# Kernel tuning notes

Measured on AMD Instinct MI355X. Metric: run time of the kernel, lower is better.

## Reference

```python
import jax, jax.numpy as jnp
import numpy as np

T, N, E, NNZ, F, D = 8, 50000, 5000, 100000, 128, 128


def setup_inputs() -> dict:
    key = jax.random.key(0)
    ks = jax.random.split(key, 5)
    x = jax.random.normal(ks[0], (T, N, F), jnp.float32)
    pair_nodes = jax.random.randint(ks[1], (T, NNZ), 0, N)
    pair_edges = jax.random.randint(ks[2], (T, NNZ), 0, E)
    W0 = jax.random.normal(ks[3], (F, D), jnp.float32) / np.sqrt(F).astype(np.float32)
    b0 = jnp.zeros((D,), jnp.float32)
    W1 = jax.random.normal(ks[4], (D, D), jnp.float32) / np.sqrt(D).astype(np.float32)
    b1 = jnp.zeros((D,), jnp.float32)
    return {"x": x, "W0": W0, "b0": b0, "W1": W1, "b1": b1,
            "pair_nodes": pair_nodes, "pair_edges": pair_edges}


def _smooth(x, pn, pe):
    """HGNN Laplacian smoothing: D_v^{-1/2} H D_e^{-1} H^T D_v^{-1/2} x.

    x: [N, D]; pn/pe: [NNZ] incidence pairs (node idx, hyperedge idx).
    """
    ones = jnp.ones(pn.shape, x.dtype)
    dv = jax.ops.segment_sum(ones, pn, num_segments=N)  # node degree
    de = jax.ops.segment_sum(ones, pe, num_segments=E)  # hyperedge degree
    dv_safe = jnp.where(dv > 0, dv, 1.0)
    de_safe = jnp.where(de > 0, de, 1.0)
    dv_isqrt = jnp.where(dv > 0, jax.lax.rsqrt(dv_safe), 0.0)
    de_inv = jnp.where(de > 0, 1.0 / de_safe, 0.0)
    xs = x * dv_isqrt[:, None]
    # node -> hyperedge gather/aggregate
    ef = jax.ops.segment_sum(xs[pn], pe, num_segments=E) * de_inv[:, None]
    # hyperedge -> node gather/scatter
    return jax.ops.segment_sum(ef[pe], pn, num_segments=N) * dv_isqrt[:, None]


def reference(x, W0, b0, W1, b1, pair_nodes, pair_edges):
    def step(xt, pn, pe):
        h = jax.nn.relu(_smooth(xt @ W0 + b0, pn, pe))   # layer 0
        h = jax.nn.relu(_smooth(h @ W1 + b1, pn, pe))    # layer 1
        return h.mean(axis=0)                            # mean pool over nodes
    tokens = jax.vmap(step)(x, pair_nodes, pair_edges)   # [T, D]
    return tokens[None]                                  # [1, T, D]
```

## Files before the change

kernel.cpp:

```cpp
#include <hip/hip_runtime.h>

#define TT  8
#define NN  50000
#define EE  5000
#define NZ  100000
#define DD  128
#define ETILES ((EE + 63) / 64)
#define NCAP 16
#define NCH 8
#define CDIV 6250
#define CCAP 16
#define LSTR 136

typedef __attribute__((ext_vector_type(8))) short short8v;
typedef __attribute__((ext_vector_type(4))) float float4v;

__device__ __forceinline__ unsigned short f2bf(float f) {
    return __builtin_bit_cast(unsigned short, (__bf16)f);
}
__device__ __forceinline__ float bf2f(unsigned short u) {
    return (float)__builtin_bit_cast(__bf16, u);
}
__device__ __forceinline__ unsigned short f2h(float f) {
    return __builtin_bit_cast(unsigned short, (_Float16)f);
}
__device__ __forceinline__ float h2f(unsigned short u) {
    return (float)__builtin_bit_cast(_Float16, u);
}

__global__ __launch_bounds__(256) void k_build(const int* __restrict__ pn, const int* __restrict__ pe,
                                               int* __restrict__ dvcnt, int* __restrict__ ccnt,
                                               unsigned short* __restrict__ ell_n,
                                               unsigned short* __restrict__ ell_ec) {
    const int t = blockIdx.x & 7;
    const int i0 = (blockIdx.x >> 3) * 1024 + threadIdx.x;
    int nv[4], ev[4];
    #pragma unroll
    for (int q = 0; q < 4; q++) {
        int i = i0 + q * 256;
        nv[q] = (i < NZ) ? pn[(size_t)t * NZ + i] : -1;
        ev[q] = (i < NZ) ? pe[(size_t)t * NZ + i] : 0;
    }
    for (int c = 0; c < NCH; c++) {
        #pragma unroll
        for (int q = 0; q < 4; q++) {
            int n = nv[q];
            if (n >= 0 && (n / CDIV) == c) {
                int e = ev[q];
                int sn = atomicAdd(&dvcnt[(size_t)t * NN + n], 1);
                if (sn < NCAP) ell_n[((size_t)t * NN + n) * NCAP + sn] = (unsigned short)e;
                int sc = atomicAdd(&ccnt[((size_t)t * EE + e) * NCH + c], 1);
                if (sc < CCAP)
                    ell_ec[(((size_t)t * EE + e) * NCH + c) * CCAP + sc] = (unsigned short)(n - c * CDIV);
            }
        }
    }
}

__global__ __launch_bounds__(256) void k_fin(const int* __restrict__ dvcnt, const int* __restrict__ ccnt,
                                             float* __restrict__ dvis, float* __restrict__ deinv) {
    int i = blockIdx.x * 256 + threadIdx.x;
    if (i < TT * NN) {
        int c = dvcnt[i];
        dvis[i] = (c > 0) ? rsqrtf((float)c) : 0.0f;
    } else {
        int j = i - TT * NN;
        if (j < TT * EE) {
            int de = 0;
            #pragma unroll
            for (int c = 0; c < NCH; c++) de += ccnt[(size_t)j * NCH + c];
            deinv[j] = (de > 0) ? 1.0f / (float)de : 0.0f;
        }
    }
}

__global__ __launch_bounds__(256) void k_prepw(const float* __restrict__ W0, const float* __restrict__ W1,
                                               unsigned short* __restrict__ fragH,
                                               unsigned short* __restrict__ fragL) {
    const float* W = blockIdx.x ? W1 : W0;
    unsigned short* fh = fragH + (size_t)blockIdx.x * 16384;
    unsigned short* fl = fragL + (size_t)blockIdx.x * 16384;
    const int wave = threadIdx.x >> 6, lane = threadIdx.x & 63;
    const int l15 = lane & 15, l4 = lane >> 4;
    #pragma unroll
    for (int c = 0; c < 2; c++)
        #pragma unroll
        for (int s = 0; s < 4; s++)
            #pragma unroll
            for (int j = 0; j < 8; j++) {
                float wv = W[(size_t)(s * 32 + l4 * 8 + j) * DD + wave * 32 + c * 16 + l15];
                unsigned short h = f2bf(wv);
                int idx = (((wave * 2 + c) * 4 + s) * 64 + lane) * 8 + j;
                fh[idx] = h;
                fl[idx] = f2bf(wv - bf2f(h));
            }
}

__global__ __launch_bounds__(256) void k_ge0(const float* __restrict__ x,
                                             const unsigned short* __restrict__ ell_ec,
                                             const int* __restrict__ ccnt,
                                             const float* __restrict__ dvis,
                                             float* __restrict__ g, float* __restrict__ se) {
    const int t = blockIdx.x & 7;
    const int e = (blockIdx.x >> 3) * 16 + (threadIdx.x >> 4);
    const int lane16 = threadIdx.x & 15;
    if (e >= EE) return;
    const float* xsrc = x + (size_t)t * NN * DD;
    const float* dvs = dvis + (size_t)t * NN;
    const int* cb = ccnt + ((size_t)t * EE + e) * NCH;
    const unsigned short* lb = ell_ec + ((size_t)t * EE + e) * NCH * CCAP;
    float acc[8] = {};
    float sacc = 0.f;
    for (int c = 0; c < NCH; c++) {
        int cnt = cb[c];
        cnt = cnt < CCAP ? cnt : CCAP;
        if (cnt == 0) continue;
        int nbase = c * CDIV;
        int idx = (lane16 < cnt) ? (nbase + (int)lb[c * CCAP + lane16]) : 0;
        float dvl = (lane16 < cnt) ? dvs[idx] : 0.f;
        sacc += dvl;
        for (int j = 0; j < cnt; j++) {
            int n = __shfl(idx, j, 16);
            float dvn = __shfl(dvl, j, 16);
            const float* xr = xsrc + (size_t)n * DD + lane16 * 8;
            float4 a0 = *(const float4*)(xr);
            float4 a1 = *(const float4*)(xr + 4);
            acc[0] += dvn * a0.x; acc[1] += dvn * a0.y; acc[2] += dvn * a0.z; acc[3] += dvn * a0.w;
            acc[4] += dvn * a1.x; acc[5] += dvn * a1.y; acc[6] += dvn * a1.z; acc[7] += dvn * a1.w;
        }
    }
    float* gout = g + ((size_t)t * EE + e) * DD;
    *(float4*)(gout + lane16 * 8)     = make_float4(acc[0], acc[1], acc[2], acc[3]);
    *(float4*)(gout + lane16 * 8 + 4) = make_float4(acc[4], acc[5], acc[6], acc[7]);
    #pragma unroll
    for (int w = 1; w < 16; w <<= 1) sacc += __shfl_xor(sacc, w, 16);
    if (lane16 == 0) se[(size_t)t * EE + e] = sacc;
}

__global__ __launch_bounds__(256) void k_gemmE(const float* __restrict__ g,
                                               const float* __restrict__ se,
                                               const float* __restrict__ deinv,
                                               const unsigned short* __restrict__ fragH,
                                               const unsigned short* __restrict__ fragL,
                                               const float* __restrict__ bias,
                                               unsigned short* __restrict__ ef) {
    __shared__ unsigned short Ah[64 * LSTR];
    __shared__ unsigned short Al[64 * LSTR];
    __shared__ unsigned short E_lds[64 * LSTR];
    const int t = blockIdx.x & 7;
    const int tile = blockIdx.x >> 3;
    const int row0 = tile * 64;
    const float* gsrc = g + (size_t)t * EE * DD;
    const float* sesrc = se + (size_t)t * EE;
    const float* desrc = deinv + (size_t)t * EE;
    unsigned short* outp = ef + (size_t)t * EE * DD;
    const int tid = threadIdx.x;
    const int wave = tid >> 6, lane = tid & 63;
    const int l15 = lane & 15, l4 = lane >> 4;

    #pragma unroll
    for (int it = 0; it < 8; it++) {
        int idx = it * 256 + tid;
        int row = idx >> 5, col4 = idx & 31;
        float4 a = make_float4(0.f, 0.f, 0.f, 0.f);
        if (row0 + row < EE) a = *(const float4*)(gsrc + (size_t)(row0 + row) * DD + col4 * 4);
        unsigned short hx = f2bf(a.x), hy = f2bf(a.y), hz = f2bf(a.z), hw = f2bf(a.w);
        *(uint2*)(&Ah[row * LSTR + col4 * 4]) = make_uint2(
            (unsigned)hx | ((unsigned)hy << 16), (unsigned)hz | ((unsigned)hw << 16));
        *(uint2*)(&Al[row * LSTR + col4 * 4]) = make_uint2(
            (unsigned)f2bf(a.x - bf2f(hx)) | ((unsigned)f2bf(a.y - bf2f(hy)) << 16),
            (unsigned)f2bf(a.z - bf2f(hz)) | ((unsigned)f2bf(a.w - bf2f(hw)) << 16));
    }

    short8v wh[2][4], wl[2][4];
    #pragma unroll
    for (int c = 0; c < 2; c++)
        #pragma unroll
        for (int s = 0; s < 4; s++) {
            int base = (((wave * 2 + c) * 4 + s) * 64 + lane) * 8;
            wh[c][s] = *(const short8v*)(fragH + base);
            wl[c][s] = *(const short8v*)(fragL + base);
        }
    __syncthreads();

    float4v acc[4][2] = {};
    #pragma unroll
    for (int s = 0; s < 4; s++)
        #pragma unroll
        for (int r = 0; r < 4; r++) {
            short8v ah = *(const short8v*)(&Ah[(r * 16 + l15) * LSTR + s * 32 + l4 * 8]);
            short8v al = *(const short8v*)(&Al[(r * 16 + l15) * LSTR + s * 32 + l4 * 8]);
            #pragma unroll
            for (int c = 0; c < 2; c++) {
                acc[r][c] = __builtin_amdgcn_mfma_f32_16x16x32_bf16(ah, wh[c][s], acc[r][c], 0, 0, 0);
                acc[r][c] = __builtin_amdgcn_mfma_f32_16x16x32_bf16(al, wh[c][s], acc[r][c], 0, 0, 0);
                acc[r][c] = __builtin_amdgcn_mfma_f32_16x16x32_bf16(ah, wl[c][s], acc[r][c], 0, 0, 0);
            }
        }

    float b2[2] = { bias[wave * 32 + l15], bias[wave * 32 + 16 + l15] };
    __syncthreads();
    #pragma unroll
    for (int r = 0; r < 4; r++) {
        int rloc = r * 16 + l4 * 4;
        if (row0 + rloc < EE) {
            float4 de4 = *(const float4*)(desrc + row0 + rloc);
            float4 se4 = *(const float4*)(sesrc + row0 + rloc);
            float dev[4] = {de4.x, de4.y, de4.z, de4.w};
            float sev[4] = {se4.x, se4.y, se4.z, se4.w};
            #pragma unroll
            for (int c = 0; c < 2; c++)
                #pragma unroll
                for (int q = 0; q < 4; q++)
                    E_lds[(rloc + q) * LSTR + wave * 32 + c * 16 + l15] =
                        f2h(dev[q] * (acc[r][c][q] + sev[q] * b2[c]));
        }
    }
    __syncthreads();
    #pragma unroll
    for (int it = 0; it < 8; it++) {
        int idx = it * 256 + tid;
        int row = idx >> 5, col4 = idx & 31;
        if (row0 + row < EE) {
            unsigned u0 = *(const unsigned*)(&E_lds[row * LSTR + col4 * 4]);
            unsigned u1 = *(const unsigned*)(&E_lds[row * LSTR + col4 * 4 + 2]);
            unsigned o2[2] = {u0, u1};
            *(uint2*)(outp + (size_t)(row0 + row) * DD + col4 * 4) = *(uint2*)o2;
        }
    }
}

__global__ __launch_bounds__(256) void k_n0(const unsigned short* __restrict__ ef,
                                            const unsigned short* __restrict__ ell_n,
                                            const int* __restrict__ dvcnt,
                                            const float* __restrict__ dvis,
                                            unsigned short* __restrict__ h) {
    const int t = blockIdx.x & 7;
    const int n = (blockIdx.x >> 3) * 16 + (threadIdx.x >> 4);
    const int lane16 = threadIdx.x & 15;
    if (n >= NN) return;
    int cn = dvcnt[(size_t)t * NN + n];
    cn = cn < NCAP ? cn : NCAP;
    float dvn = dvis[(size_t)t * NN + n];
    const unsigned short* esrc = ef + (size_t)t * EE * DD;
    int e_l = (lane16 < cn) ? (int)ell_n[((size_t)t * NN + n) * NCAP + lane16] : 0;
    float hacc[8] = {};
    for (int j = 0; j < cn; j++) {
        int e = __shfl(e_l, j, 16);
        short8v v = *(const short8v*)(esrc + (size_t)e * DD + lane16 * 8);
        #pragma unroll
        for (int k = 0; k < 8; k++) hacc[k] += h2f((unsigned short)v[k]);
    }
    short8v o;
    #pragma unroll
    for (int k = 0; k < 8; k++) o[k] = (short)f2h(dvn * fmaxf(dvn * hacc[k], 0.f));
    *(short8v*)(h + ((size_t)t * NN + n) * DD + lane16 * 8) = o;
}

__global__ __launch_bounds__(256) void k_ge1(const unsigned short* __restrict__ h,
                                             const unsigned short* __restrict__ ell_ec,
                                             const int* __restrict__ ccnt,
                                             float* __restrict__ g2) {
    const int t = blockIdx.x & 7;
    const int e = (blockIdx.x >> 3) * 16 + (threadIdx.x >> 4);
    const int lane16 = threadIdx.x & 15;
    if (e >= EE) return;
    const unsigned short* hsrc = h + (size_t)t * NN * DD;
    const int* cb = ccnt + ((size_t)t * EE + e) * NCH;
    const unsigned short* lb = ell_ec + ((size_t)t * EE + e) * NCH * CCAP;
    float acc[8] = {};
    for (int c = 0; c < NCH; c++) {
        int cnt = cb[c];
        cnt = cnt < CCAP ? cnt : CCAP;
        if (cnt == 0) continue;
        int nbase = c * CDIV;
        int idx = (lane16 < cnt) ? (nbase + (int)lb[c * CCAP + lane16]) : 0;
        for (int j = 0; j < cnt; j++) {
            int n = __shfl(idx, j, 16);
            short8v v = *(const short8v*)(hsrc + (size_t)n * DD + lane16 * 8);
            #pragma unroll
            for (int k = 0; k < 8; k++) acc[k] += h2f((unsigned short)v[k]);
        }
    }
    float* gout = g2 + ((size_t)t * EE + e) * DD;
    *(float4*)(gout + lane16 * 8)     = make_float4(acc[0], acc[1], acc[2], acc[3]);
    *(float4*)(gout + lane16 * 8 + 4) = make_float4(acc[4], acc[5], acc[6], acc[7]);
}

__global__ __launch_bounds__(256) void k_n1(const unsigned short* __restrict__ ell_n,
                                            const int* __restrict__ dvcnt,
                                            const unsigned short* __restrict__ ef,
                                            const float* __restrict__ dvis,
                                            float* __restrict__ outp) {
    const int t = blockIdx.x & 7;
    const int nbase = (blockIdx.x >> 3) * 128 + (threadIdx.x >> 4) * 8;
    const int gg_ = threadIdx.x >> 4;
    const int lane16 = threadIdx.x & 15;
    const unsigned short* esrc = ef + (size_t)t * EE * DD;
    float px[8] = {};
    #pragma unroll
    for (int i = 0; i < 8; i++) {
        int n = nbase + i;
        if (n < NN) {
            int cnt = dvcnt[(size_t)t * NN + n];
            cnt = cnt < NCAP ? cnt : NCAP;
            float dvn = dvis[(size_t)t * NN + n];
            float acc[8] = {};
            int idx = (lane16 < cnt) ? (int)ell_n[((size_t)t * NN + n) * NCAP + lane16] : 0;
            #pragma unroll
            for (int j = 0; j < 16; j++) {
                if (j < cnt) {
                    int e = __shfl(idx, j, 16);
                    short8v v = *(const short8v*)(esrc + (size_t)e * DD + lane16 * 8);
                    #pragma unroll
                    for (int k = 0; k < 8; k++) acc[k] += h2f((unsigned short)v[k]);
                }
            }
            #pragma unroll
            for (int k = 0; k < 8; k++) px[k] += fmaxf(acc[k] * dvn, 0.f);
        }
    }
    __shared__ float sp[16][128];
    #pragma unroll
    for (int k = 0; k < 8; k++) sp[gg_][lane16 * 8 + k] = px[k];
    __syncthreads();
    if (threadIdx.x < 128) {
        float ssum = 0.f;
        #pragma unroll
        for (int q = 0; q < 16; q++) ssum += sp[q][threadIdx.x];
        atomicAdd(outp + (size_t)t * DD + threadIdx.x, ssum * (1.0f / (float)NN));
    }
}

extern "C" void kernel_launch(void* const* d_in, const int* in_sizes, int n_in,
                              void* d_out, int out_size, void* d_ws, size_t ws_size,
                              hipStream_t stream) {
    const float* x  = (const float*)d_in[0];
    const float* W0 = (const float*)d_in[1];
    const float* b0 = (const float*)d_in[2];
    const float* W1 = (const float*)d_in[3];
    const float* b1 = (const float*)d_in[4];
    const int*   pn = (const int*)d_in[5];
    const int*   pe = (const int*)d_in[6];
    float* out = (float*)d_out;

    char* p = (char*)d_ws;
    auto alloc = [&](size_t bytes) -> char* {
        char* r = p;
        p += (bytes + 255) / 256 * 256;
        return r;
    };
    float* dvis  = (float*)alloc((size_t)TT * NN * 4);
    float* deinv = (float*)alloc((size_t)TT * EE * 4);
    int*   dvcnt = (int*)alloc((size_t)TT * (NN + EE * NCH) * 4);
    int*   ccnt  = dvcnt + (size_t)TT * NN;
    unsigned short* ell_n  = (unsigned short*)alloc((size_t)TT * NN * NCAP * 2);
    unsigned short* ell_ec = (unsigned short*)alloc((size_t)TT * EE * NCH * CCAP * 2);
    unsigned short* wfragH = (unsigned short*)alloc(2 * 16384 * 2);
    unsigned short* wfragL = (unsigned short*)alloc(2 * 16384 * 2);
    float* gbuf  = (float*)alloc((size_t)TT * EE * DD * 4);
    float* sebuf = (float*)alloc((size_t)TT * EE * 4);
    unsigned short* ef = (unsigned short*)alloc((size_t)TT * EE * DD * 2);
    unsigned short* h  = (unsigned short*)alloc((size_t)TT * NN * DD * 2);

    hipMemsetAsync(dvcnt, 0, (size_t)TT * (NN + EE * NCH) * 4, stream);
    hipMemsetAsync(d_out, 0, (size_t)out_size * 4, stream);

    k_prepw<<<2, 256, 0, stream>>>(W0, W1, wfragH, wfragL);
    k_build<<<((NZ + 1023) / 1024) * 8, 256, 0, stream>>>(pn, pe, dvcnt, ccnt, ell_n, ell_ec);
    k_fin<<<(TT * (NN + EE) + 255) / 256, 256, 0, stream>>>(dvcnt, ccnt, dvis, deinv);

    const dim3 ge(((EE + 15) / 16) * 8), gn(((NN + 15) / 16) * 8);

    k_ge0<<<ge, 256, 0, stream>>>(x, ell_ec, ccnt, dvis, gbuf, sebuf);
    k_gemmE<<<ETILES * 8, 256, 0, stream>>>(gbuf, sebuf, deinv, wfragH, wfragL, b0, ef);
    k_n0<<<gn, 256, 0, stream>>>(ef, ell_n, dvcnt, dvis, h);
    k_ge1<<<ge, 256, 0, stream>>>(h, ell_ec, ccnt, gbuf);
    k_gemmE<<<ETILES * 8, 256, 0, stream>>>(gbuf, sebuf, deinv, wfragH + 16384, wfragL + 16384, b1, ef);
    k_n1<<<((NN + 127) / 128) * 8, 256, 0, stream>>>(ell_n, dvcnt, ef, dvis, out);
}
```

Measured before the change: 302.8 us.

## Fold weight prep and degree finalization into neighbouring kernels, drop launches

Merges the weight-fragment preparation into extra blocks of the incidence build kernel, and removes the separate degree finalization kernel. Node inverse-sqrt degrees are now computed inline from the raw counts, and hyperedge inverse degrees are computed in the first gather kernel. This saves two kernel launches and the dvis array traffic. The node gather kernel also handles four nodes per 16-lane group with a smaller grid. In exchange it recomputes rsqrt at each use and adds some extra work to k_ge0.

```diff
diff --git a/kernel.cpp b/kernel.cpp
--- a/kernel.cpp
+++ b/kernel.cpp
@@ -11,6 +11,7 @@
 #define CDIV 6250
 #define CCAP 16
 #define LSTR 136
+#define GB (((NZ + 1023) / 1024) * 8)
 
 typedef __attribute__((ext_vector_type(8))) short short8v;
 typedef __attribute__((ext_vector_type(4))) float float4v;
@@ -31,7 +32,31 @@
 __global__ __launch_bounds__(256) void k_build(const int* __restrict__ pn, const int* __restrict__ pe,
                                                int* __restrict__ dvcnt, int* __restrict__ ccnt,
                                                unsigned short* __restrict__ ell_n,
-                                               unsigned short* __restrict__ ell_ec) {
+                                               unsigned short* __restrict__ ell_ec,
+                                               const float* __restrict__ W0, const float* __restrict__ W1,
+                                               unsigned short* __restrict__ fragH,
+                                               unsigned short* __restrict__ fragL) {
+    if (blockIdx.x >= GB) {
+        const int w = blockIdx.x - GB;
+        const float* W = w ? W1 : W0;
+        unsigned short* fh = fragH + (size_t)w * 16384;
+        unsigned short* fl = fragL + (size_t)w * 16384;
+        const int wave = threadIdx.x >> 6, lane = threadIdx.x & 63;
+        const int l15 = lane & 15, l4 = lane >> 4;
+        #pragma unroll
+        for (int c = 0; c < 2; c++)
+            #pragma unroll
+            for (int s = 0; s < 4; s++)
+                #pragma unroll
+                for (int j = 0; j < 8; j++) {
+                    float wv = W[(size_t)(s * 32 + l4 * 8 + j) * DD + wave * 32 + c * 16 + l15];
+                    unsigned short h = f2bf(wv);
+                    int idx = (((wave * 2 + c) * 4 + s) * 64 + lane) * 8 + j;
+                    fh[idx] = h;
+                    fl[idx] = f2bf(wv - bf2f(h));
+                }
+        return;
+    }
     const int t = blockIdx.x & 7;
     const int i0 = (blockIdx.x >> 3) * 1024 + threadIdx.x;
     int nv[4], ev[4];
@@ -57,67 +82,31 @@
     }
 }
 
-__global__ __launch_bounds__(256) void k_fin(const int* __restrict__ dvcnt, const int* __restrict__ ccnt,
-                                             float* __restrict__ dvis, float* __restrict__ deinv) {
-    int i = blockIdx.x * 256 + threadIdx.x;
-    if (i < TT * NN) {
-        int c = dvcnt[i];
-        dvis[i] = (c > 0) ? rsqrtf((float)c) : 0.0f;
-    } else {
-        int j = i - TT * NN;
-        if (j < TT * EE) {
-            int de = 0;
-            #pragma unroll
-            for (int c = 0; c < NCH; c++) de += ccnt[(size_t)j * NCH + c];
-            deinv[j] = (de > 0) ? 1.0f / (float)de : 0.0f;
-        }
-    }
-}
-
-__global__ __launch_bounds__(256) void k_prepw(const float* __restrict__ W0, const float* __restrict__ W1,
-                                               unsigned short* __restrict__ fragH,
-                                               unsigned short* __restrict__ fragL) {
-    const float* W = blockIdx.x ? W1 : W0;
-    unsigned short* fh = fragH + (size_t)blockIdx.x * 16384;
-    unsigned short* fl = fragL + (size_t)blockIdx.x * 16384;
-    const int wave = threadIdx.x >> 6, lane = threadIdx.x & 63;
-    const int l15 = lane & 15, l4 = lane >> 4;
-    #pragma unroll
-    for (int c = 0; c < 2; c++)
-        #pragma unroll
-        for (int s = 0; s < 4; s++)
-            #pragma unroll
-            for (int j = 0; j < 8; j++) {
-                float wv = W[(size_t)(s * 32 + l4 * 8 + j) * DD + wave * 32 + c * 16 + l15];
-                unsigned short h = f2bf(wv);
-                int idx = (((wave * 2 + c) * 4 + s) * 64 + lane) * 8 + j;
-                fh[idx] = h;
-                fl[idx] = f2bf(wv - bf2f(h));
-            }
-}
-
 __global__ __launch_bounds__(256) void k_ge0(const float* __restrict__ x,
                                              const unsigned short* __restrict__ ell_ec,
                                              const int* __restrict__ ccnt,
-                                             const float* __restrict__ dvis,
-                                             float* __restrict__ g, float* __restrict__ se) {
+                                             const int* __restrict__ dvcnt,
+                                             float* __restrict__ g, float* __restrict__ se,
+                                             float* __restrict__ deinv) {
     const int t = blockIdx.x & 7;
     const int e = (blockIdx.x >> 3) * 16 + (threadIdx.x >> 4);
     const int lane16 = threadIdx.x & 15;
     if (e >= EE) return;
     const float* xsrc = x + (size_t)t * NN * DD;
-    const float* dvs = dvis + (size_t)t * NN;
+    const int* dvc = dvcnt + (size_t)t * NN;
     const int* cb = ccnt + ((size_t)t * EE + e) * NCH;
     const unsigned short* lb = ell_ec + ((size_t)t * EE + e) * NCH * CCAP;
     float acc[8] = {};
     float sacc = 0.f;
+    int de = 0;
     for (int c = 0; c < NCH; c++) {
-        int cnt = cb[c];
-        cnt = cnt < CCAP ? cnt : CCAP;
+        int raw = cb[c];
+        de += raw;
+        int cnt = raw < CCAP ? raw : CCAP;
         if (cnt == 0) continue;
         int nbase = c * CDIV;
         int idx = (lane16 < cnt) ? (nbase + (int)lb[c * CCAP + lane16]) : 0;
-        float dvl = (lane16 < cnt) ? dvs[idx] : 0.f;
+        float dvl = (lane16 < cnt) ? rsqrtf((float)dvc[idx]) : 0.f;
         sacc += dvl;
         for (int j = 0; j < cnt; j++) {
             int n = __shfl(idx, j, 16);
@@ -134,7 +123,10 @@
     *(float4*)(gout + lane16 * 8 + 4) = make_float4(acc[4], acc[5], acc[6], acc[7]);
     #pragma unroll
     for (int w = 1; w < 16; w <<= 1) sacc += __shfl_xor(sacc, w, 16);
-    if (lane16 == 0) se[(size_t)t * EE + e] = sacc;
+    if (lane16 == 0) {
+        se[(size_t)t * EE + e] = sacc;
+        deinv[(size_t)t * EE + e] = (de > 0) ? 1.0f / (float)de : 0.0f;
+    }
 }
 
 __global__ __launch_bounds__(256) void k_gemmE(const float* __restrict__ g,
@@ -233,28 +225,32 @@
 __global__ __launch_bounds__(256) void k_n0(const unsigned short* __restrict__ ef,
                                             const unsigned short* __restrict__ ell_n,
                                             const int* __restrict__ dvcnt,
-                                            const float* __restrict__ dvis,
                                             unsigned short* __restrict__ h) {
     const int t = blockIdx.x & 7;
-    const int n = (blockIdx.x >> 3) * 16 + (threadIdx.x >> 4);
+    const int nb0 = (blockIdx.x >> 3) * 64;
+    const int gg = threadIdx.x >> 4;
     const int lane16 = threadIdx.x & 15;
-    if (n >= NN) return;
-    int cn = dvcnt[(size_t)t * NN + n];
-    cn = cn < NCAP ? cn : NCAP;
-    float dvn = dvis[(size_t)t * NN + n];
     const unsigned short* esrc = ef + (size_t)t * EE * DD;
-    int e_l = (lane16 < cn) ? (int)ell_n[((size_t)t * NN + n) * NCAP + lane16] : 0;
-    float hacc[8] = {};
-    for (int j = 0; j < cn; j++) {
-        int e = __shfl(e_l, j, 16);
-        short8v v = *(const short8v*)(esrc + (size_t)e * DD + lane16 * 8);
-        #pragma unroll
-        for (int k = 0; k < 8; k++) hacc[k] += h2f((unsigned short)v[k]);
-    }
-    short8v o;
-    #pragma unroll
-    for (int k = 0; k < 8; k++) o[k] = (short)f2h(dvn * fmaxf(dvn * hacc[k], 0.f));
-    *(short8v*)(h + ((size_t)t * NN + n) * DD + lane16 * 8) = o;
+    #pragma unroll
+    for (int i = 0; i < 4; i++) {
+        int n = nb0 + i * 16 + gg;
+        if (n >= NN) break;
+        int craw = dvcnt[(size_t)t * NN + n];
+        int cn = craw < NCAP ? craw : NCAP;
+        float dvn = (craw > 0) ? rsqrtf((float)craw) : 0.0f;
+        int e_l = (lane16 < cn) ? (int)ell_n[((size_t)t * NN + n) * NCAP + lane16] : 0;
+        float hacc[8] = {};
+        for (int j = 0; j < cn; j++) {
+            int e = __shfl(e_l, j, 16);
+            short8v v = *(const short8v*)(esrc + (size_t)e * DD + lane16 * 8);
+            #pragma unroll
+            for (int k = 0; k < 8; k++) hacc[k] += h2f((unsigned short)v[k]);
+        }
+        short8v o;
+        #pragma unroll
+        for (int k = 0; k < 8; k++) o[k] = (short)f2h(dvn * fmaxf(dvn * hacc[k], 0.f));
+        *(short8v*)(h + ((size_t)t * NN + n) * DD + lane16 * 8) = o;
+    }
 }
 
 __global__ __launch_bounds__(256) void k_ge1(const unsigned short* __restrict__ h,
@@ -290,7 +286,6 @@
 __global__ __launch_bounds__(256) void k_n1(const unsigned short* __restrict__ ell_n,
                                             const int* __restrict__ dvcnt,
                                             const unsigned short* __restrict__ ef,
-                                            const float* __restrict__ dvis,
                                             float* __restrict__ outp) {
     const int t = blockIdx.x & 7;
     const int nbase = (blockIdx.x >> 3) * 128 + (threadIdx.x >> 4) * 8;
@@ -302,9 +297,9 @@
     for (int i = 0; i < 8; i++) {
         int n = nbase + i;
         if (n < NN) {
-            int cnt = dvcnt[(size_t)t * NN + n];
-            cnt = cnt < NCAP ? cnt : NCAP;
-            float dvn = dvis[(size_t)t * NN + n];
+            int craw = dvcnt[(size_t)t * NN + n];
+            int cnt = craw < NCAP ? craw : NCAP;
+            float dvn = (craw > 0) ? rsqrtf((float)craw) : 0.0f;
             float acc[8] = {};
             int idx = (lane16 < cnt) ? (int)ell_n[((size_t)t * NN + n) * NCAP + lane16] : 0;
             #pragma unroll
@@ -350,8 +345,6 @@
         p += (bytes + 255) / 256 * 256;
         return r;
     };
-    float* dvis  = (float*)alloc((size_t)TT * NN * 4);
-    float* deinv = (float*)alloc((size_t)TT * EE * 4);
     int*   dvcnt = (int*)alloc((size_t)TT * (NN + EE * NCH) * 4);
     int*   ccnt  = dvcnt + (size_t)TT * NN;
     unsigned short* ell_n  = (unsigned short*)alloc((size_t)TT * NN * NCAP * 2);
@@ -360,22 +353,22 @@
     unsigned short* wfragL = (unsigned short*)alloc(2 * 16384 * 2);
     float* gbuf  = (float*)alloc((size_t)TT * EE * DD * 4);
     float* sebuf = (float*)alloc((size_t)TT * EE * 4);
+    float* deinv = (float*)alloc((size_t)TT * EE * 4);
     unsigned short* ef = (unsigned short*)alloc((size_t)TT * EE * DD * 2);
     unsigned short* h  = (unsigned short*)alloc((size_t)TT * NN * DD * 2);
 
     hipMemsetAsync(dvcnt, 0, (size_t)TT * (NN + EE * NCH) * 4, stream);
     hipMemsetAsync(d_out, 0, (size_t)out_size * 4, stream);
 
-    k_prepw<<<2, 256, 0, stream>>>(W0, W1, wfragH, wfragL);
-    k_build<<<((NZ + 1023) / 1024) * 8, 256, 0, stream>>>(pn, pe, dvcnt, ccnt, ell_n, ell_ec);
-    k_fin<<<(TT * (NN + EE) + 255) / 256, 256, 0, stream>>>(dvcnt, ccnt, dvis, deinv);
-
-    const dim3 ge(((EE + 15) / 16) * 8), gn(((NN + 15) / 16) * 8);
-
-    k_ge0<<<ge, 256, 0, stream>>>(x, ell_ec, ccnt, dvis, gbuf, sebuf);
+    k_build<<<GB + 2, 256, 0, stream>>>(pn, pe, dvcnt, ccnt, ell_n, ell_ec,
+                                        W0, W1, wfragH, wfragL);
+
+    const dim3 ge(((EE + 15) / 16) * 8);
+
+    k_ge0<<<ge, 256, 0, stream>>>(x, ell_ec, ccnt, dvcnt, gbuf, sebuf, deinv);
     k_gemmE<<<ETILES * 8, 256, 0, stream>>>(gbuf, sebuf, deinv, wfragH, wfragL, b0, ef);
-    k_n0<<<gn, 256, 0, stream>>>(ef, ell_n, dvcnt, dvis, h);
+    k_n0<<<((NN + 63) / 64) * 8, 256, 0, stream>>>(ef, ell_n, dvcnt, h);
     k_ge1<<<ge, 256, 0, stream>>>(h, ell_ec, ccnt, gbuf);
     k_gemmE<<<ETILES * 8, 256, 0, stream>>>(gbuf, sebuf, deinv, wfragH + 16384, wfragL + 16384, b1, ef);
-    k_n1<<<((NN + 127) / 128) * 8, 256, 0, stream>>>(ell_n, dvcnt, ef, dvis, out);
-}
+    k_n1<<<((NN + 127) / 128) * 8, 256, 0, stream>>>(ell_n, dvcnt, ef, out);
+}
```

Result: no change. 301.7 us (-0.4%).
